# Kernel optimization log

Hardware: AMD Instinct MI355X
Metric: run time of the kernel (lower is better)

The kernel has to match this reference:

```python
import jax, jax.numpy as jnp
import numpy as np

EPS = 1e-8


def box2corners(box):
    # box: (B,N,5) = x,y,w,h,alpha -> corners (B,N,4,2), CCW template
    x, y, w, h, alpha = (box[..., i] for i in range(5))
    tx = jnp.array([0.5, -0.5, -0.5, 0.5], dtype=box.dtype)
    ty = jnp.array([0.5, 0.5, -0.5, -0.5], dtype=box.dtype)
    x_off = w[..., None] * tx          # (B,N,4)
    y_off = h[..., None] * ty
    c = jnp.cos(alpha)[..., None]
    s = jnp.sin(alpha)[..., None]
    cx = x[..., None] + c * x_off - s * y_off
    cy = y[..., None] + s * x_off + c * y_off
    return jnp.stack([cx, cy], axis=-1)


def box_intersection(corners1, corners2):
    # all pairwise edge intersections: (B,N,4,4,2) points + (B,N,4,4) mask
    line1 = jnp.concatenate([corners1, jnp.roll(corners1, -1, axis=2)], axis=-1)
    line2 = jnp.concatenate([corners2, jnp.roll(corners2, -1, axis=2)], axis=-1)
    l1 = line1[:, :, :, None, :]   # (B,N,4,1,4)
    l2 = line2[:, :, None, :, :]   # (B,N,1,4,4)
    x1, y1, x2, y2 = (l1[..., i] for i in range(4))
    x3, y3, x4, y4 = (l2[..., i] for i in range(4))
    num = (y4 - y3) * (x2 - x1) - (x4 - x3) * (y2 - y1)
    den_t = (x4 - x3) * (y1 - y3) - (y4 - y3) * (x1 - x3)
    den_u = (x2 - x1) * (y1 - y3) - (y2 - y1) * (x1 - x3)
    safe = jnp.where(num == 0., 1., num)
    t = jnp.where(num == 0., -1., den_t / safe)
    u = jnp.where(num == 0., -1., -den_u / safe)
    mask = (t > 0.) & (t < 1.) & (u > 0.) & (u < 1.)
    px = x1 + t * (x2 - x1)
    py = y1 + t * (y2 - y1)
    pts = jnp.stack([px, py], axis=-1) * mask[..., None].astype(corners1.dtype)
    return pts, mask


def box1_in_box2(corners1, corners2):
    # which corners of box1 lie inside box2 -> (B,N,4) bool
    a = corners2[:, :, 0:1, :]
    b = corners2[:, :, 1:2, :]
    d = corners2[:, :, 3:4, :]
    ab, ad, am = b - a, d - a, corners1 - a
    p_ab = jnp.sum(ab * am, axis=-1)
    p_ad = jnp.sum(ad * am, axis=-1)
    n_ab = jnp.sum(ab * ab, axis=-1)
    n_ad = jnp.sum(ad * ad, axis=-1)
    eps = 1e-6
    c1 = (p_ab / n_ab > -eps) & (p_ab / n_ab < 1. + eps)
    c2 = (p_ad / n_ad > -eps) & (p_ad / n_ad < 1. + eps)
    return c1 & c2


def oriented_box_intersection_2d(corners1, corners2):
    # intersection area of two rotated boxes via vertex sort + shoelace
    inters, m_int = box_intersection(corners1, corners2)       # (B,N,4,4,2)
    c1_in_2 = box1_in_box2(corners1, corners2)                 # (B,N,4)
    c2_in_1 = box1_in_box2(corners2, corners1)
    B, N = corners1.shape[0], corners1.shape[1]
    verts = jnp.concatenate([corners1, corners2,
                             inters.reshape(B, N, 16, 2)], axis=2)  # (B,N,24,2)
    mask = jnp.concatenate([c1_in_2, c2_in_1,
                            m_int.reshape(B, N, 16)], axis=2)       # (B,N,24)
    maskf = mask.astype(verts.dtype)
    nv = jnp.sum(mask, axis=-1)                                # (B,N) int, num valid
    mean = (jnp.sum(verts * maskf[..., None], axis=2, keepdims=True)
            / jnp.maximum(nv[..., None, None].astype(verts.dtype), 1.))
    rel = verts - mean
    ang = jnp.where(mask, jnp.arctan2(rel[..., 1], rel[..., 0]), 1e6)
    order = jnp.argsort(ang, axis=-1)                          # valid CCW, invalid last
    sorted_v = jnp.take_along_axis(verts, order[..., None], axis=2)
    # pad invalid slots with first valid vertex: zero shoelace contribution
    sel = jnp.arange(24)[None, None, :] < nv[..., None]
    poly = jnp.where(sel[..., None], sorted_v, sorted_v[:, :, 0:1, :])
    nxt = jnp.roll(poly, -1, axis=2)
    area = 0.5 * jnp.abs(jnp.sum(poly[..., 0] * nxt[..., 1]
                                 - nxt[..., 0] * poly[..., 1], axis=-1))
    return area


def diff_iou_rotated_3d(box3d1, box3d2):
    # boxes: (B,N,7) = x,y,z,dx,dy,dz,yaw
    idx = jnp.array([0, 1, 3, 4, 6])
    c1 = box2corners(box3d1[..., idx])
    c2 = box2corners(box3d2[..., idx])
    inter_2d = oriented_box_intersection_2d(c1, c2)
    zmax1 = box3d1[..., 2] + box3d1[..., 5] * 0.5
    zmin1 = box3d1[..., 2] - box3d1[..., 5] * 0.5
    zmax2 = box3d2[..., 2] + box3d2[..., 5] * 0.5
    zmin2 = box3d2[..., 2] - box3d2[..., 5] * 0.5
    z_overlap = jnp.clip(jnp.minimum(zmax1, zmax2) - jnp.maximum(zmin1, zmin2), 0.)
    inter_3d = inter_2d * z_overlap
    v1 = box3d1[..., 3] * box3d1[..., 4] * box3d1[..., 5]
    v2 = box3d2[..., 3] * box3d2[..., 4] * box3d2[..., 5]
    union = v1 + v2 - inter_3d
    return inter_3d / union


def setup_inputs() -> dict:
    key = jax.random.key(0)
    k1, k2, k3, k4, k5 = jax.random.split(key, 5)
    N = 500000
    ctr = jax.random.uniform(k1, (N, 3), minval=-40., maxval=40.)
    dims = jax.random.uniform(k2, (N, 3), minval=1., maxval=5.)
    yaw = jax.random.uniform(k3, (N, 1), minval=-np.pi, maxval=np.pi)
    pred = jnp.concatenate([ctr, dims, yaw], axis=-1).astype(jnp.float32)
    noise = jax.random.normal(k4, (N, 7), dtype=jnp.float32) * jnp.array(
        [0.5, 0.5, 0.3, 0.3, 0.3, 0.3, 0.2], dtype=jnp.float32)
    target = pred + noise
    target = target.at[:, 3:6].set(jnp.maximum(target[:, 3:6], 0.5))
    weight = jax.random.uniform(k5, (N,), dtype=jnp.float32)
    return {"pred": pred, "target": target, "weight": weight}


def reference(pred, target, weight):
    loss_weight = 1.0
    target = jnp.where(jnp.isnan(target), pred, target)
    iou = diff_iou_rotated_3d(pred[None], target[None])        # (1,N)
    loss = 1. - iou
    loss = loss * weight[None]
    return loss_weight * jnp.mean(loss)
```

## Files before the change

### kernel.cpp

```cpp
#include <hip/hip_runtime.h>
#include <hip/hip_fp16.h>
#include <math.h>

#define THREADS 64
#define VSTRIDE 25

__device__ __forceinline__ float prcp(float x) { return __builtin_amdgcn_rcpf(x); }

__device__ __forceinline__ unsigned packh2(float x, float y) {
    __half2 h = __floats2half2_rn(x, y);
    return *reinterpret_cast<unsigned*>(&h);
}
__device__ __forceinline__ void unpackh2(unsigned u, float& x, float& y) {
    __half2 h = *reinterpret_cast<__half2*>(&u);
    x = __low2float(h); y = __high2float(h);
}

__global__ void __launch_bounds__(THREADS) iou3d_kernel(
    const float* __restrict__ pred, const float* __restrict__ tgt,
    const float* __restrict__ wgt, float* __restrict__ partial, int N) {
    __shared__ unsigned ldsbuf[THREADS * VSTRIDE];
    int tid = threadIdx.x;
    unsigned* myv = &ldsbuf[tid * VSTRIDE];
    int n = blockIdx.x * THREADS + tid;
    float loss = 0.0f;
    if (n < N) {
        float p[7], t[7];
#pragma unroll
        for (int k = 0; k < 7; k++) {
            p[k] = pred[(size_t)n * 7 + k];
            float tv = tgt[(size_t)n * 7 + k];
            t[k] = (tv != tv) ? p[k] : tv;
        }
        float w = wgt[n];
        float zmax1 = p[2] + p[5] * 0.5f, zmin1 = p[2] - p[5] * 0.5f;
        float zmax2 = t[2] + t[5] * 0.5f, zmin2 = t[2] - t[5] * 0.5f;
        float zov = fmaxf(fminf(zmax1, zmax2) - fmaxf(zmin1, zmin2), 0.0f);
        float vol1 = p[3] * p[4] * p[5], vol2 = t[3] * t[4] * t[5];

        float hw1 = 0.5f * p[3], hh1 = 0.5f * p[4];
        float hw2 = 0.5f * t[3], hh2 = 0.5f * t[4];
        float s1, c1v, s2, c2v;
        __sincosf(p[6], &s1, &c1v);
        __sincosf(t[6], &s2, &c2v);
        float c12 = c1v * c2v + s1 * s2;
        float s12 = s1 * c2v - c1v * s2;
        float ddx = p[0] - t[0], ddy = p[1] - t[1];
        float T12x =  c2v * ddx + s2 * ddy;
        float T12y = -s2 * ddx + c2v * ddy;
        float T21x = -(c1v * ddx + s1 * ddy);
        float T21y =  s1 * ddx - c1v * ddy;
        float ux = c12 * hw1, uy = s12 * hw1;
        float wx = -s12 * hh1, wy = c12 * hh1;
        float fx[4], fy[4];
        fx[0] = T12x + ux + wx; fy[0] = T12y + uy + wy;
        fx[1] = T12x - ux + wx; fy[1] = T12y - uy + wy;
        fx[2] = T12x - ux - wx; fy[2] = T12y - uy - wy;
        fx[3] = T12x + ux - wx; fy[3] = T12y + uy - wy;

        unsigned vm = 0;
        float bx2 = hw2 * (1.0f + 2e-6f), by2 = hh2 * (1.0f + 2e-6f);
#pragma unroll
        for (int k = 0; k < 4; k++) {
            bool c = (fabsf(fx[k]) < bx2) && (fabsf(fy[k]) < by2);
            vm |= ((unsigned)c) << k;
        }
        float u2x = c12 * hw2, u2y = -s12 * hw2;
        float v2x = s12 * hh2, v2y = c12 * hh2;
        float bx1 = hw1 * (1.0f + 2e-6f), by1 = hh1 * (1.0f + 2e-6f);
        {
            float qx, qy;
            qx = T21x + u2x + v2x; qy = T21y + u2y + v2y;
            vm |= ((unsigned)((fabsf(qx) < bx1) && (fabsf(qy) < by1))) << 4;
            qx = T21x - u2x + v2x; qy = T21y - u2y + v2y;
            vm |= ((unsigned)((fabsf(qx) < bx1) && (fabsf(qy) < by1))) << 5;
            qx = T21x - u2x - v2x; qy = T21y - u2y - v2y;
            vm |= ((unsigned)((fabsf(qx) < bx1) && (fabsf(qy) < by1))) << 6;
            qx = T21x + u2x - v2x; qy = T21y + u2y - v2y;
            vm |= ((unsigned)((fabsf(qx) < bx1) && (fabsf(qy) < by1))) << 7;
        }
        float sx = 0.0f, sy = 0.0f;
#pragma unroll
        for (int k = 0; k < 4; k++) {
            myv[k] = packh2(fx[k], fy[k]);
            bool v = (vm >> k) & 1u;
            sx += v ? fx[k] : 0.0f; sy += v ? fy[k] : 0.0f;
        }
        myv[4] = packh2(hw2, hh2);  myv[5] = packh2(-hw2, hh2);
        myv[6] = packh2(-hw2, -hh2); myv[7] = packh2(hw2, -hh2);
        {
            bool v4 = (vm >> 4) & 1u, v5 = (vm >> 5) & 1u, v6 = (vm >> 6) & 1u, v7 = (vm >> 7) & 1u;
            sx += (v4 ? hw2 : 0.0f) + (v5 ? -hw2 : 0.0f) + (v6 ? -hw2 : 0.0f) + (v7 ? hw2 : 0.0f);
            sy += (v4 ? hh2 : 0.0f) + (v5 ? hh2 : 0.0f) + (v6 ? -hh2 : 0.0f) + (v7 ? -hh2 : 0.0f);
        }

        float tux = ux + ux, tuy = uy + uy, twx = wx + wx, twy = wy + wy;
        float rtux = prcp(tux), rtuy = prcp(tuy), rtwx = prcp(twx), rtwy = prcp(twy);
        float dxe[4] = {-tux, -twx, tux, twx};
        float dye[4] = {-tuy, -twy, tuy, twy};
        float rdxe[4] = {-rtux, -rtwx, rtux, rtwx};
        float rdye[4] = {-rtuy, -rtwy, rtuy, rtwy};
        float r2w = prcp(hw2 + hw2), r2h = prcp(hh2 + hh2);

        float pvar[16];
#pragma unroll
        for (int e1 = 0; e1 < 4; e1++) {
            float x1 = fx[e1], y1 = fy[e1];
            {
                float tt = (hh2 - y1) * rdye[e1];
                float px = fmaf(tt, dxe[e1], x1);
                float uu = (hw2 - px) * (-r2w);
                bool mk = (tt > 0.0f) && (tt < 1.0f) && (uu > 0.0f) && (uu < 1.0f);
                pvar[e1 * 4 + 0] = px;
                float pxm = mk ? px : 0.0f, pym = mk ? hh2 : 0.0f;
                myv[8 + e1 * 4 + 0] = packh2(pxm, pym);
                sx += pxm; sy += pym;
                vm |= ((unsigned)mk) << (8 + e1 * 4 + 0);
            }
            {
                float tt = (-hw2 - x1) * rdxe[e1];
                float py = fmaf(tt, dye[e1], y1);
                float uu = (hh2 - py) * (-r2h);
                bool mk = (tt > 0.0f) && (tt < 1.0f) && (uu > 0.0f) && (uu < 1.0f);
                pvar[e1 * 4 + 1] = py;
                float pxm = mk ? -hw2 : 0.0f, pym = mk ? py : 0.0f;
                myv[8 + e1 * 4 + 1] = packh2(pxm, pym);
                sx += pxm; sy += pym;
                vm |= ((unsigned)mk) << (8 + e1 * 4 + 1);
            }
            {
                float tt = (-hh2 - y1) * rdye[e1];
                float px = fmaf(tt, dxe[e1], x1);
                float uu = (-hw2 - px) * r2w;
                bool mk = (tt > 0.0f) && (tt < 1.0f) && (uu > 0.0f) && (uu < 1.0f);
                pvar[e1 * 4 + 2] = px;
                float pxm = mk ? px : 0.0f, pym = mk ? -hh2 : 0.0f;
                myv[8 + e1 * 4 + 2] = packh2(pxm, pym);
                sx += pxm; sy += pym;
                vm |= ((unsigned)mk) << (8 + e1 * 4 + 2);
            }
            {
                float tt = (hw2 - x1) * rdxe[e1];
                float py = fmaf(tt, dye[e1], y1);
                float uu = (-hh2 - py) * r2h;
                bool mk = (tt > 0.0f) && (tt < 1.0f) && (uu > 0.0f) && (uu < 1.0f);
                pvar[e1 * 4 + 3] = py;
                float pxm = mk ? hw2 : 0.0f, pym = mk ? py : 0.0f;
                myv[8 + e1 * 4 + 3] = packh2(pxm, pym);
                sx += pxm; sy += pym;
                vm |= ((unsigned)mk) << (8 + e1 * 4 + 3);
            }
        }

        int nv = __popc(vm);
        float r0 = prcp(fmaxf((float)nv, 1.0f));
        float mx = sx * r0, my = sy * r0;

        unsigned ka[24];
#define MKKEY(K, XR, YR) do { \
        float xr_ = (XR), yr_ = (YR); \
        float d_ = fabsf(xr_) + fabsf(yr_); \
        float q_ = 1.0f - xr_ * prcp(d_); \
        float pa_ = copysignf(q_, yr_) + 4.0f; \
        unsigned key_ = (__float_as_uint(pa_) & 0xFFFFFFE0u) | (unsigned)(K); \
        ka[K] = ((vm >> (K)) & 1u) ? key_ : (0x7F000000u | (unsigned)(K)); \
    } while (0)
        float hpx = hw2 - mx, hmx = -hw2 - mx, hpy = hh2 - my, hmy = -hh2 - my;
#pragma unroll
        for (int k = 0; k < 4; k++) MKKEY(k, fx[k] - mx, fy[k] - my);
        MKKEY(4, hpx, hpy); MKKEY(5, hmx, hpy); MKKEY(6, hmx, hmy); MKKEY(7, hpx, hmy);
#pragma unroll
        for (int e1 = 0; e1 < 4; e1++) {
            MKKEY(8 + e1 * 4 + 0, pvar[e1 * 4 + 0] - mx, hpy);
            MKKEY(8 + e1 * 4 + 1, hmx, pvar[e1 * 4 + 1] - my);
            MKKEY(8 + e1 * 4 + 2, pvar[e1 * 4 + 2] - mx, hmy);
            MKKEY(8 + e1 * 4 + 3, hpx, pvar[e1 * 4 + 3] - my);
        }
#undef MKKEY

#define CE(A, B) { unsigned lo_ = ka[A] < ka[B] ? ka[A] : ka[B]; \
                   unsigned hi_ = ka[A] < ka[B] ? ka[B] : ka[A]; \
                   ka[A] = lo_; ka[B] = hi_; }
        CE(0,1); CE(2,3); CE(4,5); CE(6,7); CE(8,9); CE(10,11); CE(12,13); CE(14,15); CE(16,17); CE(18,19); CE(20,21); CE(22,23);
        CE(0,2); CE(1,3); CE(4,6); CE(5,7); CE(8,10); CE(9,11); CE(12,14); CE(13,15); CE(16,18); CE(17,19); CE(20,22); CE(21,23);
        CE(1,2); CE(5,6); CE(9,10); CE(13,14); CE(17,18); CE(21,22);
        CE(0,4); CE(1,5); CE(2,6); CE(3,7); CE(8,12); CE(9,13); CE(10,14); CE(11,15); CE(16,20); CE(17,21); CE(18,22); CE(19,23);
        CE(2,4); CE(3,5); CE(10,12); CE(11,13); CE(18,20); CE(19,21);
        CE(1,2); CE(3,4); CE(5,6); CE(9,10); CE(11,12); CE(13,14); CE(17,18); CE(19,20); CE(21,22);
        CE(0,8); CE(1,9); CE(2,10); CE(3,11); CE(4,12); CE(5,13); CE(6,14); CE(7,15);
        CE(4,8); CE(5,9); CE(6,10); CE(7,11);
        CE(2,4); CE(3,5); CE(6,8); CE(7,9); CE(10,12); CE(11,13); CE(18,20); CE(19,21);
        CE(1,2); CE(3,4); CE(5,6); CE(7,8); CE(9,10); CE(11,12); CE(13,14); CE(17,18); CE(19,20); CE(21,22);
        CE(0,16); CE(1,17); CE(2,18); CE(3,19); CE(4,20); CE(5,21); CE(6,22); CE(7,23);
        CE(8,16); CE(9,17); CE(10,18); CE(11,19); CE(12,20); CE(13,21); CE(14,22); CE(15,23);
        CE(4,8); CE(5,9); CE(6,10); CE(7,11); CE(12,16); CE(13,17); CE(14,18); CE(15,19);
        CE(2,4); CE(3,5); CE(6,8); CE(7,9); CE(10,12); CE(11,13); CE(14,16); CE(15,17); CE(18,20); CE(19,21);
        CE(1,2); CE(3,4); CE(5,6); CE(7,8); CE(9,10); CE(11,12); CE(13,14); CE(15,16); CE(17,18); CE(19,20); CE(21,22);
#undef CE

        unsigned gu[24];
#pragma unroll
        for (int i = 0; i < 24; i++) gu[i] = myv[ka[i] & 31u];
        float g0x, g0y;
        unpackh2(gu[0], g0x, g0y);
        float prevx = g0x, prevy = g0y;
        float area2 = 0.0f;
#pragma unroll
        for (int i = 1; i < 24; i++) {
            float xx, yy;
            unpackh2(gu[i], xx, yy);
            bool c = i < nv;
            float cxv = c ? xx : g0x;
            float cyv = c ? yy : g0y;
            area2 += prevx * cyv - cxv * prevy;
            prevx = cxv; prevy = cyv;
        }
        area2 += prevx * g0y - g0x * prevy;
        float inter2d = 0.5f * fabsf(area2);

        float inter3d = inter2d * zov;
        float uni = vol1 + vol2 - inter3d;
        float iou = inter3d / uni;
        loss = (1.0f - iou) * w;
    }

#pragma unroll
    for (int off = 32; off > 0; off >>= 1) loss += __shfl_down(loss, off, 64);
    if (threadIdx.x == 0) partial[blockIdx.x] = loss;
}

__global__ void __launch_bounds__(1024) reduce_kernel(const float* __restrict__ partial,
                                                      int nb, float* __restrict__ out, int N) {
    float s = 0.0f;
    for (int i = threadIdx.x; i < nb; i += 1024) s += partial[i];
#pragma unroll
    for (int off = 32; off > 0; off >>= 1) s += __shfl_down(s, off, 64);
    __shared__ float sm[16];
    int lane = threadIdx.x & 63, wv = threadIdx.x >> 6;
    if (lane == 0) sm[wv] = s;
    __syncthreads();
    if (threadIdx.x == 0) {
        float tot = 0.0f;
#pragma unroll
        for (int k = 0; k < 16; k++) tot += sm[k];
        out[0] = tot / (float)N;
    }
}

extern "C" void kernel_launch(void* const* d_in, const int* in_sizes, int n_in,
                              void* d_out, int out_size, void* d_ws, size_t ws_size,
                              hipStream_t stream) {
    const float* pred = (const float*)d_in[0];
    const float* tgt  = (const float*)d_in[1];
    const float* wgt  = (const float*)d_in[2];
    int N = in_sizes[2];
    int nb = (N + THREADS - 1) / THREADS;
    float* partial = (float*)d_ws;
    iou3d_kernel<<<nb, THREADS, 0, stream>>>(pred, tgt, wgt, partial, N);
    reduce_kernel<<<1, 1024, 0, stream>>>(partial, nb, (float*)d_out, N);
}
```

Baseline: 28.76 us.

## Sort vertex payloads in registers, drop LDS, fuse reduction via atomics

Vertex coordinates are no longer staged in per-thread LDS and gathered after the sort. The packed half2 coordinates now travel with the keys through the sorting network in registers, which removes the LDS traffic and the gather step. The intersection mask test uses direct coordinate comparisons instead of reciprocal-based u parameters. Blocks grow to 256 threads, and the separate reduce kernel is replaced by a memset plus a per-block atomicAdd, removing one launch. The trade-offs are higher register pressure from the doubled swaps, atomic contention on a single output, and non-deterministic summation order.

```diff
diff --git a/kernel.cpp b/kernel.cpp
--- a/kernel.cpp
+++ b/kernel.cpp
@@ -2,8 +2,7 @@
 #include <hip/hip_fp16.h>
 #include <math.h>
 
-#define THREADS 64
-#define VSTRIDE 25
+#define THREADS 256
 
 __device__ __forceinline__ float prcp(float x) { return __builtin_amdgcn_rcpf(x); }
 
@@ -18,10 +17,8 @@
 
 __global__ void __launch_bounds__(THREADS) iou3d_kernel(
     const float* __restrict__ pred, const float* __restrict__ tgt,
-    const float* __restrict__ wgt, float* __restrict__ partial, int N) {
-    __shared__ unsigned ldsbuf[THREADS * VSTRIDE];
+    const float* __restrict__ wgt, float* __restrict__ out, int N) {
     int tid = threadIdx.x;
-    unsigned* myv = &ldsbuf[tid * VSTRIDE];
     int n = blockIdx.x * THREADS + tid;
     float loss = 0.0f;
     if (n < N) {
@@ -36,7 +33,7 @@
         float zmax1 = p[2] + p[5] * 0.5f, zmin1 = p[2] - p[5] * 0.5f;
         float zmax2 = t[2] + t[5] * 0.5f, zmin2 = t[2] - t[5] * 0.5f;
         float zov = fmaxf(fminf(zmax1, zmax2) - fmaxf(zmin1, zmin2), 0.0f);
-        float vol1 = p[3] * p[4] * p[5], vol2 = t[3] * t[4] * t[5];
+        float volsum = p[3] * p[4] * p[5] + t[3] * t[4] * t[5];
 
         float hw1 = 0.5f * p[3], hh1 = 0.5f * p[4];
         float hw2 = 0.5f * t[3], hh2 = 0.5f * t[4];
@@ -82,12 +79,9 @@
         float sx = 0.0f, sy = 0.0f;
 #pragma unroll
         for (int k = 0; k < 4; k++) {
-            myv[k] = packh2(fx[k], fy[k]);
             bool v = (vm >> k) & 1u;
             sx += v ? fx[k] : 0.0f; sy += v ? fy[k] : 0.0f;
         }
-        myv[4] = packh2(hw2, hh2);  myv[5] = packh2(-hw2, hh2);
-        myv[6] = packh2(-hw2, -hh2); myv[7] = packh2(hw2, -hh2);
         {
             bool v4 = (vm >> 4) & 1u, v5 = (vm >> 5) & 1u, v6 = (vm >> 6) & 1u, v7 = (vm >> 7) & 1u;
             sx += (v4 ? hw2 : 0.0f) + (v5 ? -hw2 : 0.0f) + (v6 ? -hw2 : 0.0f) + (v7 ? hw2 : 0.0f);
@@ -100,54 +94,41 @@
         float dye[4] = {-tuy, -twy, tuy, twy};
         float rdxe[4] = {-rtux, -rtwx, rtux, rtwx};
         float rdye[4] = {-rtuy, -rtwy, rtuy, rtwy};
-        float r2w = prcp(hw2 + hw2), r2h = prcp(hh2 + hh2);
-
-        float pvar[16];
+        float w3 = 3.0f * hw2, h3 = 3.0f * hh2;
+        float pv[16];
 #pragma unroll
         for (int e1 = 0; e1 < 4; e1++) {
             float x1 = fx[e1], y1 = fy[e1];
             {
                 float tt = (hh2 - y1) * rdye[e1];
                 float px = fmaf(tt, dxe[e1], x1);
-                float uu = (hw2 - px) * (-r2w);
-                bool mk = (tt > 0.0f) && (tt < 1.0f) && (uu > 0.0f) && (uu < 1.0f);
-                pvar[e1 * 4 + 0] = px;
-                float pxm = mk ? px : 0.0f, pym = mk ? hh2 : 0.0f;
-                myv[8 + e1 * 4 + 0] = packh2(pxm, pym);
-                sx += pxm; sy += pym;
+                bool mk = (tt > 0.0f) && (tt < 1.0f) && (px > hw2) && (px < w3);
+                pv[e1 * 4 + 0] = px;
+                sx += mk ? px : 0.0f; sy += mk ? hh2 : 0.0f;
                 vm |= ((unsigned)mk) << (8 + e1 * 4 + 0);
             }
             {
                 float tt = (-hw2 - x1) * rdxe[e1];
                 float py = fmaf(tt, dye[e1], y1);
-                float uu = (hh2 - py) * (-r2h);
-                bool mk = (tt > 0.0f) && (tt < 1.0f) && (uu > 0.0f) && (uu < 1.0f);
-                pvar[e1 * 4 + 1] = py;
-                float pxm = mk ? -hw2 : 0.0f, pym = mk ? py : 0.0f;
-                myv[8 + e1 * 4 + 1] = packh2(pxm, pym);
-                sx += pxm; sy += pym;
+                bool mk = (tt > 0.0f) && (tt < 1.0f) && (py > hh2) && (py < h3);
+                pv[e1 * 4 + 1] = py;
+                sx += mk ? -hw2 : 0.0f; sy += mk ? py : 0.0f;
                 vm |= ((unsigned)mk) << (8 + e1 * 4 + 1);
             }
             {
                 float tt = (-hh2 - y1) * rdye[e1];
                 float px = fmaf(tt, dxe[e1], x1);
-                float uu = (-hw2 - px) * r2w;
-                bool mk = (tt > 0.0f) && (tt < 1.0f) && (uu > 0.0f) && (uu < 1.0f);
-                pvar[e1 * 4 + 2] = px;
-                float pxm = mk ? px : 0.0f, pym = mk ? -hh2 : 0.0f;
-                myv[8 + e1 * 4 + 2] = packh2(pxm, pym);
-                sx += pxm; sy += pym;
+                bool mk = (tt > 0.0f) && (tt < 1.0f) && (px < -hw2) && (px > -w3);
+                pv[e1 * 4 + 2] = px;
+                sx += mk ? px : 0.0f; sy += mk ? -hh2 : 0.0f;
                 vm |= ((unsigned)mk) << (8 + e1 * 4 + 2);
             }
             {
                 float tt = (hw2 - x1) * rdxe[e1];
                 float py = fmaf(tt, dye[e1], y1);
-                float uu = (-hh2 - py) * r2h;
-                bool mk = (tt > 0.0f) && (tt < 1.0f) && (uu > 0.0f) && (uu < 1.0f);
-                pvar[e1 * 4 + 3] = py;
-                float pxm = mk ? hw2 : 0.0f, pym = mk ? py : 0.0f;
-                myv[8 + e1 * 4 + 3] = packh2(pxm, pym);
-                sx += pxm; sy += pym;
+                bool mk = (tt > 0.0f) && (tt < 1.0f) && (py < -hh2) && (py > -h3);
+                pv[e1 * 4 + 3] = py;
+                sx += mk ? hw2 : 0.0f; sy += mk ? py : 0.0f;
                 vm |= ((unsigned)mk) << (8 + e1 * 4 + 3);
             }
         }
@@ -156,31 +137,33 @@
         float r0 = prcp(fmaxf((float)nv, 1.0f));
         float mx = sx * r0, my = sy * r0;
 
-        unsigned ka[24];
-#define MKKEY(K, XR, YR) do { \
+        unsigned kk[24], pp[24];
+#define MK(K, XR, YR, PX, PY) do { \
         float xr_ = (XR), yr_ = (YR); \
         float d_ = fabsf(xr_) + fabsf(yr_); \
         float q_ = 1.0f - xr_ * prcp(d_); \
         float pa_ = copysignf(q_, yr_) + 4.0f; \
         unsigned key_ = (__float_as_uint(pa_) & 0xFFFFFFE0u) | (unsigned)(K); \
-        ka[K] = ((vm >> (K)) & 1u) ? key_ : (0x7F000000u | (unsigned)(K)); \
+        kk[K] = ((vm >> (K)) & 1u) ? key_ : (0x7F000000u | (unsigned)(K)); \
+        pp[K] = packh2((PX), (PY)); \
     } while (0)
         float hpx = hw2 - mx, hmx = -hw2 - mx, hpy = hh2 - my, hmy = -hh2 - my;
 #pragma unroll
-        for (int k = 0; k < 4; k++) MKKEY(k, fx[k] - mx, fy[k] - my);
-        MKKEY(4, hpx, hpy); MKKEY(5, hmx, hpy); MKKEY(6, hmx, hmy); MKKEY(7, hpx, hmy);
+        for (int k = 0; k < 4; k++) MK(k, fx[k] - mx, fy[k] - my, fx[k], fy[k]);
+        MK(4, hpx, hpy, hw2, hh2);  MK(5, hmx, hpy, -hw2, hh2);
+        MK(6, hmx, hmy, -hw2, -hh2); MK(7, hpx, hmy, hw2, -hh2);
 #pragma unroll
         for (int e1 = 0; e1 < 4; e1++) {
-            MKKEY(8 + e1 * 4 + 0, pvar[e1 * 4 + 0] - mx, hpy);
-            MKKEY(8 + e1 * 4 + 1, hmx, pvar[e1 * 4 + 1] - my);
-            MKKEY(8 + e1 * 4 + 2, pvar[e1 * 4 + 2] - mx, hmy);
-            MKKEY(8 + e1 * 4 + 3, hpx, pvar[e1 * 4 + 3] - my);
-        }
-#undef MKKEY
-
-#define CE(A, B) { unsigned lo_ = ka[A] < ka[B] ? ka[A] : ka[B]; \
-                   unsigned hi_ = ka[A] < ka[B] ? ka[B] : ka[A]; \
-                   ka[A] = lo_; ka[B] = hi_; }
+            MK(8 + e1 * 4 + 0, pv[e1 * 4 + 0] - mx, hpy, pv[e1 * 4 + 0], hh2);
+            MK(8 + e1 * 4 + 1, hmx, pv[e1 * 4 + 1] - my, -hw2, pv[e1 * 4 + 1]);
+            MK(8 + e1 * 4 + 2, pv[e1 * 4 + 2] - mx, hmy, pv[e1 * 4 + 2], -hh2);
+            MK(8 + e1 * 4 + 3, hpx, pv[e1 * 4 + 3] - my, hw2, pv[e1 * 4 + 3]);
+        }
+#undef MK
+
+#define CE(A, B) { bool sw_ = kk[B] < kk[A]; \
+        unsigned kt_ = sw_ ? kk[B] : kk[A]; unsigned kb_ = sw_ ? kk[A] : kk[B]; kk[A] = kt_; kk[B] = kb_; \
+        unsigned pt_ = sw_ ? pp[B] : pp[A]; unsigned pb_ = sw_ ? pp[A] : pp[B]; pp[A] = pt_; pp[B] = pb_; }
         CE(0,1); CE(2,3); CE(4,5); CE(6,7); CE(8,9); CE(10,11); CE(12,13); CE(14,15); CE(16,17); CE(18,19); CE(20,21); CE(22,23);
         CE(0,2); CE(1,3); CE(4,6); CE(5,7); CE(8,10); CE(9,11); CE(12,14); CE(13,15); CE(16,18); CE(17,19); CE(20,22); CE(21,23);
         CE(1,2); CE(5,6); CE(9,10); CE(13,14); CE(17,18); CE(21,22);
@@ -198,17 +181,13 @@
         CE(1,2); CE(3,4); CE(5,6); CE(7,8); CE(9,10); CE(11,12); CE(13,14); CE(15,16); CE(17,18); CE(19,20); CE(21,22);
 #undef CE
 
-        unsigned gu[24];
-#pragma unroll
-        for (int i = 0; i < 24; i++) gu[i] = myv[ka[i] & 31u];
         float g0x, g0y;
-        unpackh2(gu[0], g0x, g0y);
-        float prevx = g0x, prevy = g0y;
-        float area2 = 0.0f;
+        unpackh2(pp[0], g0x, g0y);
+        float prevx = g0x, prevy = g0y, area2 = 0.0f;
 #pragma unroll
         for (int i = 1; i < 24; i++) {
             float xx, yy;
-            unpackh2(gu[i], xx, yy);
+            unpackh2(pp[i], xx, yy);
             bool c = i < nv;
             float cxv = c ? xx : g0x;
             float cyv = c ? yy : g0y;
@@ -219,31 +198,22 @@
         float inter2d = 0.5f * fabsf(area2);
 
         float inter3d = inter2d * zov;
-        float uni = vol1 + vol2 - inter3d;
+        float uni = volsum - inter3d;
         float iou = inter3d / uni;
         loss = (1.0f - iou) * w;
     }
 
 #pragma unroll
     for (int off = 32; off > 0; off >>= 1) loss += __shfl_down(loss, off, 64);
-    if (threadIdx.x == 0) partial[blockIdx.x] = loss;
-}
-
-__global__ void __launch_bounds__(1024) reduce_kernel(const float* __restrict__ partial,
-                                                      int nb, float* __restrict__ out, int N) {
-    float s = 0.0f;
-    for (int i = threadIdx.x; i < nb; i += 1024) s += partial[i];
-#pragma unroll
-    for (int off = 32; off > 0; off >>= 1) s += __shfl_down(s, off, 64);
-    __shared__ float sm[16];
+    __shared__ float sm[THREADS / 64];
     int lane = threadIdx.x & 63, wv = threadIdx.x >> 6;
-    if (lane == 0) sm[wv] = s;
+    if (lane == 0) sm[wv] = loss;
     __syncthreads();
     if (threadIdx.x == 0) {
-        float tot = 0.0f;
-#pragma unroll
-        for (int k = 0; k < 16; k++) tot += sm[k];
-        out[0] = tot / (float)N;
+        float s = 0.0f;
+#pragma unroll
+        for (int k = 0; k < THREADS / 64; k++) s += sm[k];
+        atomicAdd(out, s / (float)N);
     }
 }
 
@@ -255,7 +225,6 @@
     const float* wgt  = (const float*)d_in[2];
     int N = in_sizes[2];
     int nb = (N + THREADS - 1) / THREADS;
-    float* partial = (float*)d_ws;
-    iou3d_kernel<<<nb, THREADS, 0, stream>>>(pred, tgt, wgt, partial, N);
-    reduce_kernel<<<1, 1024, 0, stream>>>(partial, nb, (float*)d_out, N);
-}
+    hipMemsetAsync(d_out, 0, sizeof(float), stream);
+    iou3d_kernel<<<nb, THREADS, 0, stream>>>(pred, tgt, wgt, (float*)d_out, N);
+}
```

Measured after the change: 39.08 us. 35.9% more time.
